# Kernel optimization log

Measured on AMD Instinct MI355X. Metric: run time of the kernel, lower is better.

The kernel has to match this reference:

```python
import jax, jax.numpy as jnp
import numpy as np

H = 8   # num_heads
K = 2   # num_timescales (hard-coded in module)


def _apply_rope(x, cos, sin):
    # x: [B,T,H,D]; cos/sin: [1,T,1,D/2]; interleaved even/odd pairs
    xp = x.reshape(*x.shape[:-1], -1, 2)
    xr, xi = xp[..., 0], xp[..., 1]
    rr = xr * cos - xi * sin
    ri = xr * sin + xi * cos
    return jnp.stack([rr, ri], axis=-1).reshape(x.shape)


def setup_inputs() -> dict:
    key = jax.random.key(0)
    ks = jax.random.split(key, 11)
    B, T, C = 4, 2048, 1024
    HK = H * K
    s = 0.02  # xavier-ish scale
    return {
        'x': jax.random.normal(ks[0], (B, T, C), jnp.float32),
        'mask': jnp.ones((B, T), jnp.int32),
        'Wq': jax.random.normal(ks[1], (C, C), jnp.float32) * s,
        'Wk': jax.random.normal(ks[2], (C, C), jnp.float32) * s,
        'Wv': jax.random.normal(ks[3], (C, C), jnp.float32) * s,
        'Wb': jax.random.normal(ks[4], (C, HK), jnp.float32) * s,
        'bb': jax.random.normal(ks[5], (HK,), jnp.float32) * 0.5 + 2.0,
        'Wm': jax.random.normal(ks[6], (C, HK), jnp.float32) * s,
        'bm': jax.random.normal(ks[7], (HK,), jnp.float32) * 0.1,
        'Wo': jax.random.normal(ks[8], (C, C), jnp.float32) * s,
        'bo': jnp.zeros((C,), jnp.float32),
    }


def reference(x, mask, Wq, Wk, Wv, Wb, bb, Wm, bm, Wo, bo):
    B, T, C = x.shape
    D = C // H
    q = (x @ Wq).reshape(B, T, H, D)
    k = (x @ Wk).reshape(B, T, H, D)
    v = (x @ Wv).reshape(B, T, H, D)

    # RoPE cache
    inv_freq = 1.0 / (10000.0 ** (jnp.arange(0, D, 2, dtype=jnp.float32) / D))
    freqs = jnp.arange(T, dtype=jnp.float32)[:, None] * inv_freq[None, :]  # [T,D/2]
    cos = jnp.cos(freqs)[None, :, None, :].astype(x.dtype)
    sin = jnp.sin(freqs)[None, :, None, :].astype(x.dtype)
    q = _apply_rope(q, cos, sin)
    k = _apply_rope(k, cos, sin)

    beta = jax.nn.sigmoid((x @ Wb + bb).reshape(B, T, H, K))  # [B,T,H,K]
    mix = jax.nn.softmax((x @ Wm + bm).reshape(B, T, H, K), axis=-1)

    def step(S, ins):
        # S: [B,H,K,D,D]
        q_t, k_t, v_t, b_t, m_t, mk = ins  # [B,H,D],[B,H,D],[B,H,D],[B,H,K],[B,H,K],[B]
        outer = jnp.einsum('bhd,bhe->bhde', k_t, v_t)          # [B,H,D,D]
        S_new = b_t[..., None, None] * S + outer[:, :, None]   # [B,H,K,D,D]
        S = jnp.where(mk[:, None, None, None, None] > 0, S_new, S)
        y_k = jnp.einsum('bhd,bhkde->bhke', q_t, S)            # [B,H,K,D]
        y_t = jnp.sum(y_k * m_t[..., None], axis=2)            # [B,H,D]
        y_t = jnp.where(mk[:, None, None] > 0, y_t, jnp.zeros_like(y_t))
        return S, y_t

    S0 = jnp.zeros((B, H, K, D, D), x.dtype)
    xs = (jnp.swapaxes(q, 0, 1), jnp.swapaxes(k, 0, 1), jnp.swapaxes(v, 0, 1),
          jnp.swapaxes(beta, 0, 1), jnp.swapaxes(mix, 0, 1), mask.T)
    _, ys = jax.lax.scan(step, S0, xs)           # ys: [T,B,H,D]
    y = jnp.swapaxes(ys, 0, 1).reshape(B, T, C)
    return y @ Wo + bo
```

## Files before the change

kernel.cpp:

```cpp
#include <hip/hip_runtime.h>

typedef __attribute__((ext_vector_type(4))) float f32x4;
typedef __attribute__((ext_vector_type(8))) __bf16 bf16x8;

#define T_DIM 2048
#define B_DIM 4
#define C_DIM 1024
#define H_N 8
#define D_H 128
#define M_ROWS 8192
#define MC ((size_t)M_ROWS * C_DIM)
#define LCH 64
#define NCH (T_DIM / LCH)
#define CHSZ (128 * 128)
#define SWE(r) ((((r) ^ ((r) >> 3)) & 7) << 3)

#define GLDS16(g, l) __builtin_amdgcn_global_load_lds( \
    (const __attribute__((address_space(1))) void*)(g), \
    (__attribute__((address_space(3))) void*)(l), 16, 0, 0)

__global__ void rope_table_k(float2* __restrict__ tab) {
    int idx = blockIdx.x * 256 + threadIdx.x;
    if (idx >= T_DIM * 64) return;
    int t = idx >> 6, i = idx & 63;
    float freq = expf(-(2.0f * (float)i / 128.0f) * 9.210340371976184f);
    float a = (float)t * freq;
    tab[idx] = make_float2(cosf(a), sinf(a));
}

__global__ __launch_bounds__(256) void cvt_x_k(const float* __restrict__ in,
                                               __bf16* __restrict__ out) {
    int i = blockIdx.x * 256 + threadIdx.x;
    f32x4 a = ((const f32x4*)in)[i * 2];
    f32x4 b = ((const f32x4*)in)[i * 2 + 1];
    bf16x8 o;
    o[0] = (__bf16)a.x; o[1] = (__bf16)a.y; o[2] = (__bf16)a.z; o[3] = (__bf16)a.w;
    o[4] = (__bf16)b.x; o[5] = (__bf16)b.y; o[6] = (__bf16)b.z; o[7] = (__bf16)b.w;
    ((bf16x8*)out)[i] = o;
}

__global__ __launch_bounds__(256) void wtrans_k(
    const float* __restrict__ W0, const float* __restrict__ W1,
    const float* __restrict__ W2, const float* __restrict__ W3,
    __bf16* __restrict__ out) {
    const float* W = blockIdx.z == 0 ? W0 : blockIdx.z == 1 ? W1 :
                     blockIdx.z == 2 ? W2 : W3;
    __bf16* o = out + (size_t)blockIdx.z * C_DIM * C_DIM;
    __shared__ float t[64][65];
    int tid = threadIdx.x;
    int r0 = blockIdx.y * 64, c0 = blockIdx.x * 64;
    #pragma unroll
    for (int it = 0; it < 4; ++it) {
        int idx = it * 256 + tid;
        int r = idx >> 4, c4 = (idx & 15) * 4;
        f32x4 v = *(const f32x4*)(W + (size_t)(r0 + r) * C_DIM + c0 + c4);
        t[r][c4] = v.x; t[r][c4 + 1] = v.y; t[r][c4 + 2] = v.z; t[r][c4 + 3] = v.w;
    }
    __syncthreads();
    #pragma unroll
    for (int it = 0; it < 2; ++it) {
        int idx = it * 256 + tid;
        int n = idx >> 3, k8 = (idx & 7) * 8;
        bf16x8 ov;
        #pragma unroll
        for (int j = 0; j < 8; ++j) ov[j] = (__bf16)t[k8 + j][n];
        *(bf16x8*)(o + (size_t)(c0 + n) * C_DIM + r0 + k8) = ov;
    }
}

__global__ __launch_bounds__(256) void wbm_trans_k(
    const float* __restrict__ Wb, const float* __restrict__ Wm,
    __bf16* __restrict__ WbmT) {
    int n = blockIdx.x;
    int col = n & 15;
    const float* W = (n < 16) ? Wb : Wm;
    for (int k = threadIdx.x; k < C_DIM; k += 256)
        WbmT[(size_t)n * C_DIM + k] = (__bf16)W[(size_t)k * 16 + col];
}

__global__ __launch_bounds__(256) void betamix_mfma(
    const __bf16* __restrict__ xb, const __bf16* __restrict__ WbmT,
    const float* __restrict__ bb, const float* __restrict__ bm,
    float* __restrict__ beta, float* __restrict__ mix) {
    __shared__ __bf16 As[2][32 * 64];

    int tid = threadIdx.x;
    int w = tid >> 6, lane = tid & 63;
    int lr = lane & 15, lg = lane >> 4;
    int ifr = w >> 1, j = w & 1;
    int rows0 = blockIdx.x * 32;

    int srow = tid >> 3;
    int sg = (tid & 7) ^ (srow & 7);
    size_t aoff = (size_t)(rows0 + srow) * C_DIM + sg * 8;
    int ldso = w * 64 * 16;

    f32x4 acc = {};
    const __bf16* Wrow = WbmT + (size_t)(j * 16 + lr) * C_DIM;

    GLDS16(xb + aoff, (char*)As[0] + ldso);
    asm volatile("s_waitcnt vmcnt(0)" ::: "memory");
    __syncthreads();

    for (int t = 0; t < 16; ++t) {
        int cur = t & 1;
        if (t < 15) GLDS16(xb + aoff + (t + 1) * 64, (char*)As[cur ^ 1] + ldso);
        #pragma unroll
        for (int ss = 0; ss < 2; ++ss) {
            int ar = ifr * 16 + lr;
            bf16x8 af = *(const bf16x8*)((char*)As[cur] + ar * 128 + (((ss * 4 + lg) ^ (ar & 7)) << 4));
            bf16x8 bf = *(const bf16x8*)(Wrow + t * 64 + ss * 32 + lg * 8);
            acc = __builtin_amdgcn_mfma_f32_16x16x32_bf16(af, bf, acc, 0, 0, 0);
        }
        asm volatile("s_waitcnt vmcnt(0)" ::: "memory");
        __syncthreads();
    }

    float bias = (j ? bm : bb)[lr];
    #pragma unroll
    for (int r = 0; r < 4; ++r) {
        int row = rows0 + ifr * 16 + lg * 4 + r;
        float v = acc[r] + bias;
        if (j == 0) {
            beta[(size_t)row * 16 + lr] = 1.f / (1.f + expf(-v));
        } else {
            float other = __shfl_xor(v, 1);
            float mx = fmaxf(v, other);
            float e = expf(v - mx), eo = expf(other - mx);
            mix[(size_t)row * 16 + lr] = e / (e + eo);
        }
    }
}

template<bool ROPE, bool OUTF32>
__global__ __launch_bounds__(256) void gemm_bt(
    const __bf16* __restrict__ A, const __bf16* __restrict__ BT,
    void* __restrict__ Cp, int M, int N, int K,
    const float2* __restrict__ rope_tab, const float* __restrict__ bias) {
    __shared__ __bf16 As[2][128 * 64];
    __shared__ __bf16 Bs[2][128 * 64];

    int tid = threadIdx.x;
    int nTN = N >> 7;
    int cpx = gridDim.x >> 3;
    int bid = ((int)blockIdx.x & 7) * cpx + ((int)blockIdx.x >> 3);
    int bm = bid / nTN, bn = bid % nTN;
    int m_base = bm << 7, n_base = bn << 7;
    int w = tid >> 6, lane = tid & 63;
    int lr = lane & 15, lg = lane >> 4;
    int wm = (w >> 1) * 64, wn = (w & 1) * 64;

    size_t aoff[4], boff[4];
    int ldso[4];
    #pragma unroll
    for (int it = 0; it < 4; ++it) {
        int gi = it * 256 + tid;
        int row = gi >> 3;
        int g = (gi & 7) ^ (row & 7);
        aoff[it] = (size_t)(m_base + row) * K + g * 8;
        boff[it] = (size_t)(n_base + row) * K + g * 8;
        ldso[it] = (it * 256 + w * 64) * 16;
    }

#define STAGE_G(bufi, k0)                                                   \
    _Pragma("unroll")                                                       \
    for (int it = 0; it < 4; ++it) {                                        \
        GLDS16(A + aoff[it] + (k0), (char*)As[bufi] + ldso[it]);            \
        GLDS16(BT + boff[it] + (k0), (char*)Bs[bufi] + ldso[it]);           \
    }

    f32x4 acc[4][4] = {};

    STAGE_G(0, 0);
    asm volatile("s_waitcnt vmcnt(0)" ::: "memory");
    __syncthreads();

    int nt = K >> 6;
    for (int t = 0; t < nt; ++t) {
        int cur = t & 1;
        if (t + 1 < nt) STAGE_G(cur ^ 1, (t + 1) * 64);
        #pragma unroll
        for (int ss = 0; ss < 2; ++ss) {
            bf16x8 af[4], bfr[4];
            #pragma unroll
            for (int i = 0; i < 4; ++i) {
                int ar = wm + i * 16 + lr;
                af[i] = *(const bf16x8*)((char*)As[cur] + ar * 128 + (((ss * 4 + lg) ^ (ar & 7)) << 4));
                int br = wn + i * 16 + lr;
                bfr[i] = *(const bf16x8*)((char*)Bs[cur] + br * 128 + (((ss * 4 + lg) ^ (br & 7)) << 4));
            }
            #pragma unroll
            for (int i = 0; i < 4; ++i)
                #pragma unroll
                for (int j = 0; j < 4; ++j)
                    acc[i][j] = __builtin_amdgcn_mfma_f32_16x16x32_bf16(af[i], bfr[j], acc[i][j], 0, 0, 0);
        }
        asm volatile("s_waitcnt vmcnt(0)" ::: "memory");
        __syncthreads();
    }
#undef STAGE_G

    #pragma unroll
    for (int i = 0; i < 4; ++i) {
        #pragma unroll
        for (int j = 0; j < 4; ++j) {
            #pragma unroll
            for (int r = 0; r < 4; ++r) {
                int grow = m_base + wm + i * 16 + (lg << 2) + r;
                int gcol = n_base + wn + j * 16 + lr;
                float val = acc[i][j][r];
                if (ROPE) {
                    float partner = __shfl_xor(val, 1);
                    int t = grow & (T_DIM - 1);
                    int ii = (gcol & 127) >> 1;
                    float2 cs = rope_tab[t * 64 + ii];
                    val = (gcol & 1) ? (partner * cs.y + val * cs.x)
                                     : (val * cs.x - partner * cs.y);
                }
                if (bias) val += bias[gcol];
                size_t idx = (size_t)grow * N + gcol;
                if (OUTF32) ((float*)Cp)[idx] = val;
                else        ((__bf16*)Cp)[idx] = (__bf16)val;
            }
        }
    }
}

__global__ __launch_bounds__(256) void chunk_sum_k(
    const __bf16* __restrict__ kg, const __bf16* __restrict__ vg,
    const float* __restrict__ beta, const int* __restrict__ mask,
    __bf16* __restrict__ BT, float* __restrict__ cumLg) {
    __shared__ __bf16 KT[128 * 64];
    __shared__ __bf16 VT[128 * 64];
    __shared__ float wvf[LCH], mkf[LCH];

    int tid = threadIdx.x;
    int c = blockIdx.x, kk = blockIdx.y, bh = blockIdx.z;
    int b = bh >> 3, h = bh & 7;
    int scan = bh * 2 + kk;
    size_t rowb = (size_t)b * T_DIM + c * LCH;

    if (tid < 64) {
        int s = tid;
        size_t row = rowb + s;
        int mk = mask[row];
        float mf = mk ? 1.f : 0.f;
        float bt = mk ? beta[row * 16 + h * 2 + kk] : 1.f;
        float cum = bt;
        #pragma unroll
        for (int off = 1; off < 64; off <<= 1) {
            float p = __shfl(cum, (s >= off) ? s - off : 0);
            if (s >= off) cum *= p;
        }
        float cl = __shfl(cum, 63);
        wvf[s] = cl / cum;
        mkf[s] = mf;
        if (s == 63) cumLg[scan * NCH + c] = cum;
    }
    __syncthreads();

    #pragma unroll
    for (int it = 0; it < 4; ++it) {
        int f = tid + it * 256;
        int s = f >> 4, c8 = (f & 15) * 8;
        size_t g = (rowb + s) * C_DIM + h * D_H + c8;
        bf16x8 kv = *(const bf16x8*)(kg + g);
        bf16x8 vv = *(const bf16x8*)(vg + g);
        float ws_ = wvf[s], mf = mkf[s];
        #pragma unroll
        for (int j = 0; j < 8; ++j) {
            int d = c8 + j;
            KT[d * 64 + (s ^ SWE(d))] = (__bf16)(ws_ * (float)kv[j]);
            VT[d * 64 + (s ^ SWE(d))] = (__bf16)(mf * (float)vv[j]);
        }
    }
    __syncthreads();

    int w = tid >> 6, l = tid & 63;
    int lr = l & 15, lg = l >> 4;
    f32x4 acc[2][8] = {};
    #pragma unroll
    for (int kt = 0; kt < 2; ++kt) {
        int col = kt * 32 + lg * 8;
        bf16x8 aV[2], bK[8];
        #pragma unroll
        for (int et = 0; et < 2; ++et) {
            int e = w * 32 + et * 16 + lr;
            aV[et] = *(const bf16x8*)&VT[e * 64 + (col ^ SWE(e))];
        }
        #pragma unroll
        for (int dt = 0; dt < 8; ++dt) {
            int d = dt * 16 + lr;
            bK[dt] = *(const bf16x8*)&KT[d * 64 + (col ^ SWE(d))];
        }
        #pragma unroll
        for (int et = 0; et < 2; ++et)
            #pragma unroll
            for (int dt = 0; dt < 8; ++dt)
                acc[et][dt] = __builtin_amdgcn_mfma_f32_16x16x32_bf16(aV[et], bK[dt], acc[et][dt], 0, 0, 0);
    }

    __bf16* bout = BT + ((size_t)scan * NCH + c) * CHSZ;
    #pragma unroll
    for (int et = 0; et < 2; ++et)
        #pragma unroll
        for (int dt = 0; dt < 8; ++dt)
            #pragma unroll
            for (int r = 0; r < 4; ++r) {
                int e = w * 32 + et * 16 + lg * 4 + r;
                bout[e * 128 + dt * 16 + lr] = (__bf16)acc[et][dt][r];
            }
}

__global__ __launch_bounds__(256) void chunk_scan_k(
    __bf16* __restrict__ BT, const float* __restrict__ cumLg) {
    int bid = blockIdx.x;
    int scan = bid >> 3, part = bid & 7;
    int tid = threadIdx.x;
    int e = part * 16 + (tid >> 4);
    int d0 = (tid & 15) * 8;
    __bf16* base = BT + (size_t)scan * NCH * CHSZ + e * 128 + d0;
    const float* cl = cumLg + scan * NCH;
    float acc[8] = {};
    for (int c = 0; c < NCH; ++c) {
        bf16x8 bv = *(const bf16x8*)(base + (size_t)c * CHSZ);
        float g = cl[c];
        bf16x8 so;
        #pragma unroll
        for (int j = 0; j < 8; ++j) so[j] = (__bf16)acc[j];
        *(bf16x8*)(base + (size_t)c * CHSZ) = so;
        #pragma unroll
        for (int j = 0; j < 8; ++j) acc[j] = g * acc[j] + (float)bv[j];
    }
}

__global__ __launch_bounds__(256) void chunk_out_k(
    const __bf16* __restrict__ qg, const __bf16* __restrict__ kg,
    const __bf16* __restrict__ vg, const __bf16* __restrict__ ST,
    const float* __restrict__ beta, const float* __restrict__ mixp,
    const int* __restrict__ mask, __bf16* __restrict__ yg) {
    __shared__ __bf16 STs[2][64 * 128];
    __shared__ __bf16 VT[64 * 64];
    __shared__ __bf16 Ps[64 * 72];
    __shared__ float rcumf[2][64], qscf[2][64], mkf[64];

    int tid = threadIdx.x;
    int c = blockIdx.x, eh = blockIdx.y, bh = blockIdx.z;
    int b = bh >> 3, h = bh & 7;
    int e0 = eh * 64;
    size_t rowb = (size_t)b * T_DIM + c * LCH;
    int w = tid >> 6, l = tid & 63;
    int lr = l & 15, lg = l >> 4;

    {
        const __bf16* stb = ST + ((size_t)(bh * 2) * NCH + c) * CHSZ + (size_t)e0 * 128;
        int r = tid >> 4, gran = tid & 15;
        size_t goff = (size_t)r * 128 + ((gran ^ (r & 7)) * 8);
        #pragma unroll
        for (int kk = 0; kk < 2; ++kk) {
            const __bf16* sp = stb + (size_t)kk * NCH * CHSZ;
            #pragma unroll
            for (int it = 0; it < 4; ++it) {
                GLDS16(sp + goff + (size_t)it * 16 * 128,
                       (char*)STs[kk] + (it * 256 + w * 64) * 16);
            }
        }
    }

    if (tid < 128) {
        int s = tid & 63, kk = tid >> 6;
        size_t row = rowb + s;
        int mk = mask[row];
        float bt = mk ? beta[row * 16 + h * 2 + kk] : 1.f;
        float cum = bt;
        #pragma unroll
        for (int off = 1; off < 64; off <<= 1) {
            float p = __shfl(cum, (s >= off) ? s - off : 0);
            if (s >= off) cum *= p;
        }
        rcumf[kk][s] = 1.f / cum;
        qscf[kk][s] = cum * (mk ? mixp[row * 16 + h * 2 + kk] : 0.f);
        if (kk == 0) mkf[s] = mk ? 1.f : 0.f;
    }
    __syncthreads();

    #pragma unroll
    for (int it = 0; it < 2; ++it) {
        int f = tid + it * 256;
        int s = f >> 3, c8 = (f & 7) * 8;
        size_t g = (rowb + s) * C_DIM + h * D_H + e0 + c8;
        bf16x8 vv = *(const bf16x8*)(vg + g);
        float mf = mkf[s];
        #pragma unroll
        for (int j = 0; j < 8; ++j) {
            int el = c8 + j;
            VT[el * 64 + (s ^ SWE(el))] = (__bf16)(mf * (float)vv[j]);
        }
    }

    const __bf16* qrow = qg + (rowb + w * 16 + lr) * C_DIM + h * D_H;
    bf16x8 aQ[4];
    #pragma unroll
    for (int kt = 0; kt < 4; ++kt)
        aQ[kt] = *(const bf16x8*)(qrow + kt * 32 + lg * 8);

    const __bf16* kbase = kg + rowb * C_DIM + h * D_H;
    f32x4 Praw[4];
    #pragma unroll
    for (int st = 0; st < 4; ++st) {
        f32x4 p = {};
        #pragma unroll
        for (int kt = 0; kt < 4; ++kt) {
            bf16x8 bk = *(const bf16x8*)(kbase + (size_t)(st * 16 + lr) * C_DIM + kt * 32 + lg * 8);
            p = __builtin_amdgcn_mfma_f32_16x16x32_bf16(aQ[kt], bk, p, 0, 0, 0);
        }
        Praw[st] = p;
    }

    asm volatile("s_waitcnt vmcnt(0)" ::: "memory");
    __syncthreads();

    f32x4 yA[4] = {};
    #pragma unroll
    for (int kk = 0; kk < 2; ++kk) {
        #pragma unroll
        for (int st = 0; st < 4; ++st) {
            #pragma unroll
            for (int r = 0; r < 4; ++r) {
                int tl = w * 16 + lg * 4 + r;
                int sc = st * 16 + lr;
                float pv = (sc <= tl) ? Praw[st][r] * rcumf[kk][sc] * qscf[kk][tl] : 0.f;
                Ps[tl * 72 + sc] = (__bf16)pv;
            }
        }
        bf16x8 aP[2];
        #pragma unroll
        for (int k2 = 0; k2 < 2; ++k2)
            aP[k2] = *(const bf16x8*)&Ps[(w * 16 + lr) * 72 + k2 * 32 + lg * 8];

        __builtin_amdgcn_s_setprio(1);
        #pragma unroll
        for (int et = 0; et < 4; ++et) {
            int el = et * 16 + lr;
            f32x4 ys = {};
            #pragma unroll
            for (int kt = 0; kt < 4; ++kt) {
                bf16x8 bs = *(const bf16x8*)((char*)STs[kk] + el * 256 + (((kt * 4 + lg) ^ (el & 7)) << 4));
                ys = __builtin_amdgcn_mfma_f32_16x16x32_bf16(aQ[kt], bs, ys, 0, 0, 0);
            }
            f32x4 yp = {};
            #pragma unroll
            for (int k2 = 0; k2 < 2; ++k2) {
                bf16x8 bv = *(const bf16x8*)&VT[el * 64 + ((k2 * 32 + lg * 8) ^ SWE(el))];
                yp = __builtin_amdgcn_mfma_f32_16x16x32_bf16(aP[k2], bv, yp, 0, 0, 0);
            }
            #pragma unroll
            for (int r = 0; r < 4; ++r)
                yA[et][r] += ys[r] * qscf[kk][w * 16 + lg * 4 + r] + yp[r];
        }
        __builtin_amdgcn_s_setprio(0);
    }
    #pragma unroll
    for (int et = 0; et < 4; ++et)
        #pragma unroll
        for (int r = 0; r < 4; ++r) {
            size_t row = rowb + w * 16 + lg * 4 + r;
            yg[row * C_DIM + h * D_H + e0 + et * 16 + lr] = (__bf16)yA[et][r];
        }
}

extern "C" void kernel_launch(void* const* d_in, const int* in_sizes, int n_in,
                              void* d_out, int out_size, void* d_ws, size_t ws_size,
                              hipStream_t stream) {
    const float* x    = (const float*)d_in[0];
    const int*   mask = (const int*)d_in[1];
    const float* Wq   = (const float*)d_in[2];
    const float* Wk   = (const float*)d_in[3];
    const float* Wv   = (const float*)d_in[4];
    const float* Wb   = (const float*)d_in[5];
    const float* bb   = (const float*)d_in[6];
    const float* Wm   = (const float*)d_in[7];
    const float* bm   = (const float*)d_in[8];
    const float* Wo   = (const float*)d_in[9];
    const float* bo   = (const float*)d_in[10];
    float* out = (float*)d_out;

    __bf16* q    = (__bf16*)d_ws;
    __bf16* k    = q + MC;
    __bf16* v    = k + MC;
    __bf16* xb   = v + MC;
    __bf16* WT   = xb + MC;
    __bf16* BT   = WT + (size_t)4 * C_DIM * C_DIM;
    float* beta  = (float*)(BT + (size_t)64 * NCH * CHSZ);
    float* mixb  = beta + M_ROWS * 16;
    float* cumL  = mixb + M_ROWS * 16;
    float2* rope = (float2*)(cumL + 64 * NCH);
    __bf16* WbmT = (__bf16*)(rope + T_DIM * 64);
    __bf16* ysum = xb;

    rope_table_k<<<dim3((T_DIM * 64) / 256), dim3(256), 0, stream>>>(rope);
    cvt_x_k<<<dim3(MC / 8 / 256), dim3(256), 0, stream>>>(x, xb);
    wtrans_k<<<dim3(16, 16, 4), dim3(256), 0, stream>>>(Wq, Wk, Wv, Wo, WT);
    wbm_trans_k<<<dim3(32), dim3(256), 0, stream>>>(Wb, Wm, WbmT);
    betamix_mfma<<<dim3(M_ROWS / 32), dim3(256), 0, stream>>>(xb, WbmT, bb, bm, beta, mixb);

    const size_t CC = (size_t)C_DIM * C_DIM;
    dim3 ggrid((M_ROWS / 128) * (C_DIM / 128));
    gemm_bt<true,  false><<<ggrid, dim3(256), 0, stream>>>(xb, WT,          q,   M_ROWS, C_DIM, C_DIM, rope, nullptr);
    gemm_bt<true,  false><<<ggrid, dim3(256), 0, stream>>>(xb, WT + CC,     k,   M_ROWS, C_DIM, C_DIM, rope, nullptr);
    gemm_bt<false, false><<<ggrid, dim3(256), 0, stream>>>(xb, WT + 2 * CC, v,   M_ROWS, C_DIM, C_DIM, nullptr, nullptr);

    chunk_sum_k<<<dim3(NCH, 2, 32), dim3(256), 0, stream>>>(k, v, beta, mask, BT, cumL);
    chunk_scan_k<<<dim3(512), dim3(256), 0, stream>>>(BT, cumL);
    chunk_out_k<<<dim3(NCH, 2, 32), dim3(256), 0, stream>>>(q, k, v, BT, beta, mixb, mask, ysum);

    gemm_bt<false, true><<<ggrid, dim3(256), 0, stream>>>(ysum, WT + 3 * CC, out, M_ROWS, C_DIM, C_DIM, nullptr, bo);
}
```

Measured before the change: 232.1 us.

## Precompute chunk decay factors once and hoist chunk_out loads into registers

Adds a decay_k kernel that computes the per-chunk cumulative beta products, the masked weights, reciprocals and query scales once, and writes them to global buffers. chunk_sum_k and chunk_out_k now read these values instead of each repeating the shuffle scan. chunk_out_k also issues the V and K loads into registers before the LDS writes and MFMAs, and gets a launch-bounds occupancy hint. The rope-table and Wb/Wm transpose kernels are merged into one launch. The change adds an extra kernel launch and extra global traffic, and the masking of V is folded into the weight arrays.

Result: faster. 227.1 us (-2.2%).

```diff
diff --git a/kernel.cpp b/kernel.cpp
--- a/kernel.cpp
+++ b/kernel.cpp
@@ -19,13 +19,24 @@
     (const __attribute__((address_space(1))) void*)(g), \
     (__attribute__((address_space(3))) void*)(l), 16, 0, 0)
 
-__global__ void rope_table_k(float2* __restrict__ tab) {
-    int idx = blockIdx.x * 256 + threadIdx.x;
-    if (idx >= T_DIM * 64) return;
-    int t = idx >> 6, i = idx & 63;
-    float freq = expf(-(2.0f * (float)i / 128.0f) * 9.210340371976184f);
-    float a = (float)t * freq;
-    tab[idx] = make_float2(cosf(a), sinf(a));
+__global__ void small_prep_k(float2* __restrict__ tab,
+                             const float* __restrict__ Wb,
+                             const float* __restrict__ Wm,
+                             __bf16* __restrict__ WbmT) {
+    int bid = blockIdx.x;
+    if (bid < 512) {
+        int idx = bid * 256 + threadIdx.x;
+        int t = idx >> 6, i = idx & 63;
+        float freq = expf(-(2.0f * (float)i / 128.0f) * 9.210340371976184f);
+        float a = (float)t * freq;
+        tab[idx] = make_float2(cosf(a), sinf(a));
+    } else {
+        int n = bid - 512;
+        int col = n & 15;
+        const float* W = (n < 16) ? Wb : Wm;
+        for (int k = threadIdx.x; k < C_DIM; k += 256)
+            WbmT[(size_t)n * C_DIM + k] = (__bf16)W[(size_t)k * 16 + col];
+    }
 }
 
 __global__ __launch_bounds__(256) void cvt_x_k(const float* __restrict__ in,
@@ -68,16 +79,6 @@
     }
 }
 
-__global__ __launch_bounds__(256) void wbm_trans_k(
-    const float* __restrict__ Wb, const float* __restrict__ Wm,
-    __bf16* __restrict__ WbmT) {
-    int n = blockIdx.x;
-    int col = n & 15;
-    const float* W = (n < 16) ? Wb : Wm;
-    for (int k = threadIdx.x; k < C_DIM; k += 256)
-        WbmT[(size_t)n * C_DIM + k] = (__bf16)W[(size_t)k * 16 + col];
-}
-
 __global__ __launch_bounds__(256) void betamix_mfma(
     const __bf16* __restrict__ xb, const __bf16* __restrict__ WbmT,
     const float* __restrict__ bb, const float* __restrict__ bm,
@@ -130,6 +131,34 @@
             mix[(size_t)row * 16 + lr] = e / (e + eo);
         }
     }
+}
+
+__global__ __launch_bounds__(256) void decay_k(
+    const float* __restrict__ beta, const float* __restrict__ mixp,
+    const int* __restrict__ mask,
+    float* __restrict__ wvm, float* __restrict__ rcm,
+    float* __restrict__ qsc, float* __restrict__ cumLg) {
+    int gw = blockIdx.x * 4 + (threadIdx.x >> 6);
+    int s = threadIdx.x & 63;
+    int scan = gw >> 5, c = gw & 31;
+    int b = scan >> 4, hh = scan & 15;
+    size_t row = (size_t)b * T_DIM + c * LCH + s;
+    int mk = mask[row];
+    float mf = mk ? 1.f : 0.f;
+    float bt = mk ? beta[row * 16 + hh] : 1.f;
+    float mx = mk ? mixp[row * 16 + hh] : 0.f;
+    float cum = bt;
+    #pragma unroll
+    for (int off = 1; off < 64; off <<= 1) {
+        float p = __shfl(cum, (s >= off) ? s - off : 0);
+        if (s >= off) cum *= p;
+    }
+    float cl = __shfl(cum, 63);
+    size_t o = (size_t)scan * T_DIM + c * LCH + s;
+    wvm[o] = mf * cl / cum;
+    rcm[o] = mf / cum;
+    qsc[o] = mf * mx * cum;
+    if (s == 63) cumLg[scan * NCH + c] = cl;
 }
 
 template<bool ROPE, bool OUTF32>
@@ -228,36 +257,16 @@
 
 __global__ __launch_bounds__(256) void chunk_sum_k(
     const __bf16* __restrict__ kg, const __bf16* __restrict__ vg,
-    const float* __restrict__ beta, const int* __restrict__ mask,
-    __bf16* __restrict__ BT, float* __restrict__ cumLg) {
+    const float* __restrict__ wvm, __bf16* __restrict__ BT) {
     __shared__ __bf16 KT[128 * 64];
     __shared__ __bf16 VT[128 * 64];
-    __shared__ float wvf[LCH], mkf[LCH];
 
     int tid = threadIdx.x;
     int c = blockIdx.x, kk = blockIdx.y, bh = blockIdx.z;
     int b = bh >> 3, h = bh & 7;
     int scan = bh * 2 + kk;
     size_t rowb = (size_t)b * T_DIM + c * LCH;
-
-    if (tid < 64) {
-        int s = tid;
-        size_t row = rowb + s;
-        int mk = mask[row];
-        float mf = mk ? 1.f : 0.f;
-        float bt = mk ? beta[row * 16 + h * 2 + kk] : 1.f;
-        float cum = bt;
-        #pragma unroll
-        for (int off = 1; off < 64; off <<= 1) {
-            float p = __shfl(cum, (s >= off) ? s - off : 0);
-            if (s >= off) cum *= p;
-        }
-        float cl = __shfl(cum, 63);
-        wvf[s] = cl / cum;
-        mkf[s] = mf;
-        if (s == 63) cumLg[scan * NCH + c] = cum;
-    }
-    __syncthreads();
+    size_t wb = (size_t)scan * T_DIM + c * LCH;
 
     #pragma unroll
     for (int it = 0; it < 4; ++it) {
@@ -266,12 +275,12 @@
         size_t g = (rowb + s) * C_DIM + h * D_H + c8;
         bf16x8 kv = *(const bf16x8*)(kg + g);
         bf16x8 vv = *(const bf16x8*)(vg + g);
-        float ws_ = wvf[s], mf = mkf[s];
+        float ws_ = wvm[wb + s];
         #pragma unroll
         for (int j = 0; j < 8; ++j) {
             int d = c8 + j;
             KT[d * 64 + (s ^ SWE(d))] = (__bf16)(ws_ * (float)kv[j]);
-            VT[d * 64 + (s ^ SWE(d))] = (__bf16)(mf * (float)vv[j]);
+            VT[d * 64 + (s ^ SWE(d))] = vv[j];
         }
     }
     __syncthreads();
@@ -334,15 +343,15 @@
     }
 }
 
-__global__ __launch_bounds__(256) void chunk_out_k(
+__global__ __launch_bounds__(256, 3) void chunk_out_k(
     const __bf16* __restrict__ qg, const __bf16* __restrict__ kg,
     const __bf16* __restrict__ vg, const __bf16* __restrict__ ST,
-    const float* __restrict__ beta, const float* __restrict__ mixp,
-    const int* __restrict__ mask, __bf16* __restrict__ yg) {
+    const float* __restrict__ rcm, const float* __restrict__ qscg,
+    __bf16* __restrict__ yg) {
     __shared__ __bf16 STs[2][64 * 128];
     __shared__ __bf16 VT[64 * 64];
     __shared__ __bf16 Ps[64 * 72];
-    __shared__ float rcumf[2][64], qscf[2][64], mkf[64];
+    __shared__ float rcumf[2][64], qscf[2][64];
 
     int tid = threadIdx.x;
     int c = blockIdx.x, eh = blockIdx.y, bh = blockIdx.z;
@@ -369,51 +378,51 @@
 
     if (tid < 128) {
         int s = tid & 63, kk = tid >> 6;
-        size_t row = rowb + s;
-        int mk = mask[row];
-        float bt = mk ? beta[row * 16 + h * 2 + kk] : 1.f;
-        float cum = bt;
-        #pragma unroll
-        for (int off = 1; off < 64; off <<= 1) {
-            float p = __shfl(cum, (s >= off) ? s - off : 0);
-            if (s >= off) cum *= p;
-        }
-        rcumf[kk][s] = 1.f / cum;
-        qscf[kk][s] = cum * (mk ? mixp[row * 16 + h * 2 + kk] : 0.f);
-        if (kk == 0) mkf[s] = mk ? 1.f : 0.f;
-    }
-    __syncthreads();
-
+        size_t o = (size_t)(bh * 2 + kk) * T_DIM + c * LCH + s;
+        rcumf[kk][s] = rcm[o];
+        qscf[kk][s] = qscg[o];
+    }
+
+    bf16x8 vreg[2];
     #pragma unroll
     for (int it = 0; it < 2; ++it) {
         int f = tid + it * 256;
         int s = f >> 3, c8 = (f & 7) * 8;
-        size_t g = (rowb + s) * C_DIM + h * D_H + e0 + c8;
-        bf16x8 vv = *(const bf16x8*)(vg + g);
-        float mf = mkf[s];
+        vreg[it] = *(const bf16x8*)(vg + (rowb + s) * C_DIM + h * D_H + e0 + c8);
+    }
+
+    const __bf16* qrow = qg + (rowb + w * 16 + lr) * C_DIM + h * D_H;
+    bf16x8 aQ[4];
+    #pragma unroll
+    for (int kt = 0; kt < 4; ++kt)
+        aQ[kt] = *(const bf16x8*)(qrow + kt * 32 + lg * 8);
+
+    const __bf16* kbase = kg + rowb * C_DIM + h * D_H;
+    bf16x8 bkreg[16];
+    #pragma unroll
+    for (int st = 0; st < 4; ++st)
+        #pragma unroll
+        for (int kt = 0; kt < 4; ++kt)
+            bkreg[st * 4 + kt] = *(const bf16x8*)(kbase + (size_t)(st * 16 + lr) * C_DIM + kt * 32 + lg * 8);
+
+    #pragma unroll
+    for (int it = 0; it < 2; ++it) {
+        int f = tid + it * 256;
+        int s = f >> 3, c8 = (f & 7) * 8;
         #pragma unroll
         for (int j = 0; j < 8; ++j) {
             int el = c8 + j;
-            VT[el * 64 + (s ^ SWE(el))] = (__bf16)(mf * (float)vv[j]);
-        }
-    }
-
-    const __bf16* qrow = qg + (rowb + w * 16 + lr) * C_DIM + h * D_H;
-    bf16x8 aQ[4];
-    #pragma unroll
-    for (int kt = 0; kt < 4; ++kt)
-        aQ[kt] = *(const bf16x8*)(qrow + kt * 32 + lg * 8);
-
-    const __bf16* kbase = kg + rowb * C_DIM + h * D_H;
+            VT[el * 64 + (s ^ SWE(el))] = vreg[it][j];
+        }
+    }
+
     f32x4 Praw[4];
     #pragma unroll
     for (int st = 0; st < 4; ++st) {
         f32x4 p = {};
         #pragma unroll
-        for (int kt = 0; kt < 4; ++kt) {
-            bf16x8 bk = *(const bf16x8*)(kbase + (size_t)(st * 16 + lr) * C_DIM + kt * 32 + lg * 8);
-            p = __builtin_amdgcn_mfma_f32_16x16x32_bf16(aQ[kt], bk, p, 0, 0, 0);
-        }
+        for (int kt = 0; kt < 4; ++kt)
+            p = __builtin_amdgcn_mfma_f32_16x16x32_bf16(aQ[kt], bkreg[st * 4 + kt], p, 0, 0, 0);
         Praw[st] = p;
     }
 
@@ -494,15 +503,18 @@
     float* beta  = (float*)(BT + (size_t)64 * NCH * CHSZ);
     float* mixb  = beta + M_ROWS * 16;
     float* cumL  = mixb + M_ROWS * 16;
-    float2* rope = (float2*)(cumL + 64 * NCH);
+    float* wvm   = cumL + 64 * NCH;
+    float* rcm   = wvm + (size_t)64 * T_DIM;
+    float* qscg  = rcm + (size_t)64 * T_DIM;
+    float2* rope = (float2*)(qscg + (size_t)64 * T_DIM);
     __bf16* WbmT = (__bf16*)(rope + T_DIM * 64);
     __bf16* ysum = xb;
 
-    rope_table_k<<<dim3((T_DIM * 64) / 256), dim3(256), 0, stream>>>(rope);
+    small_prep_k<<<dim3(544), dim3(256), 0, stream>>>(rope, Wb, Wm, WbmT);
     cvt_x_k<<<dim3(MC / 8 / 256), dim3(256), 0, stream>>>(x, xb);
     wtrans_k<<<dim3(16, 16, 4), dim3(256), 0, stream>>>(Wq, Wk, Wv, Wo, WT);
-    wbm_trans_k<<<dim3(32), dim3(256), 0, stream>>>(Wb, Wm, WbmT);
     betamix_mfma<<<dim3(M_ROWS / 32), dim3(256), 0, stream>>>(xb, WbmT, bb, bm, beta, mixb);
+    decay_k<<<dim3(512), dim3(256), 0, stream>>>(beta, mixb, mask, wvm, rcm, qscg, cumL);
 
     const size_t CC = (size_t)C_DIM * C_DIM;
     dim3 ggrid((M_ROWS / 128) * (C_DIM / 128));
@@ -510,9 +522,9 @@
     gemm_bt<true,  false><<<ggrid, dim3(256), 0, stream>>>(xb, WT + CC,     k,   M_ROWS, C_DIM, C_DIM, rope, nullptr);
     gemm_bt<false, false><<<ggrid, dim3(256), 0, stream>>>(xb, WT + 2 * CC, v,   M_ROWS, C_DIM, C_DIM, nullptr, nullptr);
 
-    chunk_sum_k<<<dim3(NCH, 2, 32), dim3(256), 0, stream>>>(k, v, beta, mask, BT, cumL);
+    chunk_sum_k<<<dim3(NCH, 2, 32), dim3(256), 0, stream>>>(k, v, wvm, BT);
     chunk_scan_k<<<dim3(512), dim3(256), 0, stream>>>(BT, cumL);
-    chunk_out_k<<<dim3(NCH, 2, 32), dim3(256), 0, stream>>>(q, k, v, BT, beta, mixb, mask, ysum);
+    chunk_out_k<<<dim3(NCH, 2, 32), dim3(256), 0, stream>>>(q, k, v, BT, rcm, qscg, ysum);
 
     gemm_bt<false, true><<<ggrid, dim3(256), 0, stream>>>(ysum, WT + 3 * CC, out, M_ROWS, C_DIM, C_DIM, nullptr, bo);
 }
```
